# Kernel tuning notes

Hardware: AMD Instinct MI355X
Metric: run time of the kernel (lower is better)

## Reference

```python
import jax, jax.numpy as jnp
import numpy as np

B, S, H, E, F, TOP_K = 4, 2048, 512, 16, 1024, 2


def setup_inputs() -> dict:
    key = jax.random.key(0)
    k0, k1, k2, k3, k4 = jax.random.split(key, 5)
    scale = 0.02
    return {
        "inputs": jax.random.normal(k0, (B, S, H), dtype=jnp.float32),
        "router_w": jax.random.normal(k1, (E, H), dtype=jnp.float32) * scale,
        "gate_w": jax.random.normal(k2, (E, H, F), dtype=jnp.float32) * scale,
        "up_w": jax.random.normal(k3, (E, H, F), dtype=jnp.float32) * scale,
        "down_w": jax.random.normal(k4, (E, F, H), dtype=jnp.float32) * scale,
    }


def _moe_forward(inputs, router_w, gate_w, up_w, down_w):
    b, s, h = inputs.shape
    x = inputs.reshape(-1, h)                      # [T, H]
    T = x.shape[0]
    # --- routing: topk of logits then fp32 softmax over the k selected ---
    router_logits = x @ router_w.T                 # [T, E]
    top_vals, top_idx = jax.lax.top_k(router_logits, TOP_K)   # [T, K]
    weights = jax.nn.softmax(top_vals.astype(jnp.float32), axis=-1)  # [T, K]
    # dense combine weights: w[t, e] = routing weight if expert e selected else 0
    combine = jnp.zeros((T, router_w.shape[0]), jnp.float32)
    combine = combine.at[jnp.arange(T)[:, None], top_idx].set(weights)  # [T, E]

    # --- per-expert SwiGLU MLP, weighted combine (scan over experts) ---
    def step(acc, ew):
        wg, wu, wd, ce = ew                        # [H,F], [H,F], [F,H], [T]
        hid = jax.nn.silu(x @ wg) * (x @ wu)       # [T, F]
        y = hid @ wd                               # [T, H]
        return acc + ce[:, None] * y, None

    out0 = jnp.zeros_like(x)
    out, _ = jax.lax.scan(step, out0, (gate_w, up_w, down_w, combine.T))
    return out.reshape(b, s, h), router_logits, top_idx


def reference(inputs, router_w, gate_w, up_w, down_w):
    out, router_logits, selected_experts = _moe_forward(
        inputs, router_w, gate_w, up_w, down_w)
    return out
```

## Files before the change

### kernel.cpp

```cpp
#include <hip/hip_runtime.h>
#include <cstdint>
#include <cstddef>

#define T_TOK 8192
#define H_DIM 512
#define E_NUM 16
#define F_DIM 1024

typedef __bf16 bf16x8 __attribute__((ext_vector_type(8)));
typedef float f32x4 __attribute__((ext_vector_type(4)));

#define OFF_XBF  0UL
#define OFF_HID  8388608UL
#define OFF_GW   41943040UL
#define OFF_UW   58720256UL
#define OFF_DW   75497472UL
#define OFF_STOK 92274688UL
#define OFF_SW   92340224UL
#define OFF_TOPE 92405760UL
#define OFF_TOPW 92471296UL
#define OFF_CNT  92536832UL
#define OFF_CUR  92537856UL
#define OFF_OFFS 92538880UL

__device__ __forceinline__ unsigned short f2bf(float f) {
  union { float f; uint32_t u; } v; v.f = f;
  uint32_t r = v.u + 0x7fffu + ((v.u >> 16) & 1u);
  return (unsigned short)(r >> 16);
}

__device__ __forceinline__ void gld16(const void* g, void* l) {
  __builtin_amdgcn_global_load_lds(
      (const __attribute__((address_space(1))) unsigned int*)g,
      (__attribute__((address_space(3))) unsigned int*)l, 16, 0, 0);
}

__global__ __launch_bounds__(256) void k_router(
    const float* __restrict__ x, const float* __restrict__ rw,
    unsigned short* __restrict__ xbf, int* __restrict__ tope,
    float* __restrict__ topw) {
  const int wave = threadIdx.x >> 6, lane = threadIdx.x & 63;
  const int t = blockIdx.x * 4 + wave;
  const float4* xr = (const float4*)(x + (size_t)t * H_DIM + lane * 8);
  float4 a = xr[0], b = xr[1];
  float xi[8] = {a.x, a.y, a.z, a.w, b.x, b.y, b.z, b.w};
  uint4 o;
  o.x = (uint32_t)f2bf(xi[0]) | ((uint32_t)f2bf(xi[1]) << 16);
  o.y = (uint32_t)f2bf(xi[2]) | ((uint32_t)f2bf(xi[3]) << 16);
  o.z = (uint32_t)f2bf(xi[4]) | ((uint32_t)f2bf(xi[5]) << 16);
  o.w = (uint32_t)f2bf(xi[6]) | ((uint32_t)f2bf(xi[7]) << 16);
  *(uint4*)(xbf + (size_t)t * H_DIM + lane * 8) = o;
  float acc[E_NUM];
  #pragma unroll
  for (int e = 0; e < E_NUM; ++e) {
    const float4* wr = (const float4*)(rw + e * H_DIM + lane * 8);
    float4 wa = wr[0], wb = wr[1];
    acc[e] = xi[0]*wa.x + xi[1]*wa.y + xi[2]*wa.z + xi[3]*wa.w
           + xi[4]*wb.x + xi[5]*wb.y + xi[6]*wb.z + xi[7]*wb.w;
  }
  #pragma unroll
  for (int off = 1; off < 64; off <<= 1) {
    #pragma unroll
    for (int e = 0; e < E_NUM; ++e) acc[e] += __shfl_xor(acc[e], off);
  }
  if (lane == 0) {
    int e0 = 0; float v0 = acc[0];
    #pragma unroll
    for (int e = 1; e < E_NUM; ++e) if (acc[e] > v0) { v0 = acc[e]; e0 = e; }
    int e1 = -1; float v1 = -3.4e38f;
    #pragma unroll
    for (int e = 0; e < E_NUM; ++e) if (e != e0 && acc[e] > v1) { v1 = acc[e]; e1 = e; }
    float ee = __expf(v1 - v0);
    float inv = 1.0f / (1.0f + ee);
    tope[t*2]   = e0; tope[t*2+1] = e1;
    topw[t*2]   = inv; topw[t*2+1] = ee * inv;
  }
}

__global__ __launch_bounds__(256) void k_hist(
    const int* __restrict__ tope, int* __restrict__ counts) {
  __shared__ int lh[E_NUM];
  const int tid = threadIdx.x;
  if (tid < E_NUM) lh[tid] = 0;
  __syncthreads();
  atomicAdd(&lh[tope[blockIdx.x * 256 + tid]], 1);
  __syncthreads();
  if (tid < E_NUM) atomicAdd(&counts[tid * 16], lh[tid]);
}

__global__ void k_offsets(const int* __restrict__ counts, int* __restrict__ offs) {
  if (threadIdx.x == 0 && blockIdx.x == 0) {
    int s = 0;
    for (int e = 0; e < E_NUM; ++e) { offs[e] = s; s += counts[e * 16]; }
    offs[E_NUM] = s;
  }
}

__global__ __launch_bounds__(256) void k_scatter(
    const int* __restrict__ tope, const float* __restrict__ topw,
    const int* __restrict__ offs, int* __restrict__ cursors,
    int* __restrict__ stok, float* __restrict__ sw) {
  __shared__ int lh[E_NUM];
  __shared__ int lbase[E_NUM];
  const int tid = threadIdx.x;
  const int t = blockIdx.x * 256 + tid;
  if (tid < E_NUM) lh[tid] = 0;
  __syncthreads();
  int e0 = tope[t*2], e1 = tope[t*2+1];
  int r0 = atomicAdd(&lh[e0], 1);
  int r1 = atomicAdd(&lh[e1], 1);
  __syncthreads();
  if (tid < E_NUM) lbase[tid] = atomicAdd(&cursors[tid * 16], lh[tid]);
  __syncthreads();
  int s0 = offs[e0] + lbase[e0] + r0;
  int s1 = offs[e1] + lbase[e1] + r1;
  stok[s0] = t; sw[s0] = topw[t*2];
  stok[s1] = t; sw[s1] = topw[t*2+1];
}

__global__ __launch_bounds__(256) void k_prep_gu(
    const float* __restrict__ gw, const float* __restrict__ uw,
    unsigned short* __restrict__ gws, unsigned short* __restrict__ uws) {
  const int fx = blockIdx.x, kc = blockIdx.y, ez = blockIdx.z;
  const int e = ez >> 1;
  const float* src = ((ez & 1) ? uw : gw) + (size_t)e * H_DIM * F_DIM;
  unsigned short* dst = ((ez & 1) ? uws : gws);
  __shared__ float ls[32][132];
  const int tid = threadIdx.x;
  #pragma unroll
  for (int j = 0; j < 4; ++j) {
    int vi = tid + j * 256;
    int row = vi >> 5, c4 = (vi & 31) * 4;
    float4 v = *(const float4*)&src[(size_t)(kc*32 + row) * F_DIM + fx*128 + c4];
    ls[row][c4+0]=v.x; ls[row][c4+1]=v.y; ls[row][c4+2]=v.z; ls[row][c4+3]=v.w;
  }
  __syncthreads();
  size_t obase = (((size_t)e * 8 + fx) * 16 + kc) * 4096;
  #pragma unroll
  for (int j = 0; j < 2; ++j) {
    int oi = tid + j * 256;
    int f = oi >> 2, slot = oi & 3;
    int ks = ((slot ^ f) & 3) * 8;
    uint4 o;
    o.x = (uint32_t)f2bf(ls[ks+0][f]) | ((uint32_t)f2bf(ls[ks+1][f]) << 16);
    o.y = (uint32_t)f2bf(ls[ks+2][f]) | ((uint32_t)f2bf(ls[ks+3][f]) << 16);
    o.z = (uint32_t)f2bf(ls[ks+4][f]) | ((uint32_t)f2bf(ls[ks+5][f]) << 16);
    o.w = (uint32_t)f2bf(ls[ks+6][f]) | ((uint32_t)f2bf(ls[ks+7][f]) << 16);
    *(uint4*)&dst[obase + (size_t)oi * 8] = o;
  }
}

__global__ __launch_bounds__(256) void k_prep_dw(
    const float* __restrict__ dw, unsigned short* __restrict__ dws) {
  const int ht = blockIdx.x, kc = blockIdx.y, e = blockIdx.z;
  const float* src = dw + (size_t)e * F_DIM * H_DIM;
  __shared__ float ls[32][260];
  const int tid = threadIdx.x;
  #pragma unroll
  for (int j = 0; j < 8; ++j) {
    int vi = tid + j * 256;
    int row = vi >> 6, c4 = (vi & 63) * 4;
    float4 v = *(const float4*)&src[(size_t)(kc*32 + row) * H_DIM + ht*256 + c4];
    ls[row][c4+0]=v.x; ls[row][c4+1]=v.y; ls[row][c4+2]=v.z; ls[row][c4+3]=v.w;
  }
  __syncthreads();
  size_t obase = (((size_t)e * 2 + ht) * 32 + kc) * 8192;
  #pragma unroll
  for (int j = 0; j < 4; ++j) {
    int oi = tid + j * 256;
    int h = oi >> 2, slot = oi & 3;
    int ks = ((slot ^ h) & 3) * 8;
    uint4 o;
    o.x = (uint32_t)f2bf(ls[ks+0][h]) | ((uint32_t)f2bf(ls[ks+1][h]) << 16);
    o.y = (uint32_t)f2bf(ls[ks+2][h]) | ((uint32_t)f2bf(ls[ks+3][h]) << 16);
    o.z = (uint32_t)f2bf(ls[ks+4][h]) | ((uint32_t)f2bf(ls[ks+5][h]) << 16);
    o.w = (uint32_t)f2bf(ls[ks+6][h]) | ((uint32_t)f2bf(ls[ks+7][h]) << 16);
    *(uint4*)&dws[obase + (size_t)oi * 8] = o;
  }
}

__global__ __launch_bounds__(256, 2) void k_gateup(
    const unsigned short* __restrict__ xbf,
    const unsigned short* __restrict__ gws, const unsigned short* __restrict__ uws,
    const int* __restrict__ stok, const int* __restrict__ counts,
    const int* __restrict__ offs, unsigned short* __restrict__ hid) {
  const int e = blockIdx.z;
  const int cnt = counts[e * 16];
  const int t0 = blockIdx.y * 128;
  if (t0 >= cnt) return;
  const int base = offs[e];
  const int fx = blockIdx.x;

  __shared__ __align__(16) unsigned short sb[2][3][4096];

  const int tid = threadIdx.x;
  const int wave = tid >> 6, lane = tid & 63;
  const int l15 = lane & 15, hi = lane >> 4;
  const int wm = wave >> 1, wn = wave & 1;

  const int r0 = tid >> 2, slot = tid & 3;
  const int rr0 = min(t0 + r0, cnt - 1), rr1 = min(t0 + r0 + 64, cnt - 1);
  const char* sA0 = (const char*)xbf + (size_t)stok[base + rr0] * 1024 + ((slot ^ (r0 & 3)) * 16);
  const char* sA1 = (const char*)xbf + (size_t)stok[base + rr1] * 1024 + ((slot ^ (r0 & 3)) * 16);
  const char* sG = (const char*)gws + (((size_t)e * 8 + fx) * 16) * 8192 + tid * 16;
  const char* sU = (const char*)uws + (((size_t)e * 8 + fx) * 16) * 8192 + tid * 16;
  unsigned short* const dA = &sb[0][0][wave * 512];
  unsigned short* const dG = &sb[0][1][wave * 512];
  unsigned short* const dU = &sb[0][2][wave * 512];
  const int bufo = 3 * 4096;

  f32x4 accg[4][4] = {}; f32x4 accu[4][4] = {};

  #define STAGE_GU(b, kk) { \
    gld16(sA0 + (kk)*64, dA + (b)*bufo); \
    gld16(sA1 + (kk)*64, dA + (b)*bufo + 2048); \
    gld16(sG + (size_t)(kk)*8192, dG + (b)*bufo); \
    gld16(sG + (size_t)(kk)*8192 + 4096, dG + (b)*bufo + 2048); \
    gld16(sU + (size_t)(kk)*8192, dU + (b)*bufo); \
    gld16(sU + (size_t)(kk)*8192 + 4096, dU + (b)*bufo + 2048); }

  STAGE_GU(0, 0);
  __syncthreads();
  #pragma unroll 1
  for (int kk = 0; kk < 16; ++kk) {
    const int cur = kk & 1;
    if (kk < 15) STAGE_GU(cur ^ 1, kk + 1);
    const unsigned short* lA = &sb[cur][0][0];
    const unsigned short* lG = &sb[cur][1][0];
    const unsigned short* lU = &sb[cur][2][0];
    bf16x8 a[4], bg[4], bu[4];
    #pragma unroll
    for (int m = 0; m < 4; ++m) {
      int row = wm*64 + m*16 + l15;
      a[m] = *(const bf16x8*)((const char*)lA + row*64 + (((hi ^ row) & 3) << 4));
    }
    #pragma unroll
    for (int s = 0; s < 4; ++s) {
      int row = wn*64 + s*16 + l15;
      int o = row*64 + (((hi ^ row) & 3) << 4);
      bg[s] = *(const bf16x8*)((const char*)lG + o);
      bu[s] = *(const bf16x8*)((const char*)lU + o);
    }
    #pragma unroll
    for (int m = 0; m < 4; ++m)
      #pragma unroll
      for (int s = 0; s < 4; ++s) {
        accg[m][s] = __builtin_amdgcn_mfma_f32_16x16x32_bf16(a[m], bg[s], accg[m][s], 0, 0, 0);
        accu[m][s] = __builtin_amdgcn_mfma_f32_16x16x32_bf16(a[m], bu[s], accu[m][s], 0, 0, 0);
      }
    __syncthreads();
  }
  #undef STAGE_GU

  #pragma unroll
  for (int m = 0; m < 4; ++m)
    #pragma unroll
    for (int r = 0; r < 4; ++r) {
      int row = t0 + wm*64 + m*16 + hi*4 + r;
      if (row < cnt) {
        #pragma unroll
        for (int s = 0; s < 4; ++s) {
          float g = accg[m][s][r], u = accu[m][s][r];
          float h = g / (1.0f + __expf(-g)) * u;
          hid[(size_t)(base + row) * 1024 + fx*128 + wn*64 + s*16 + l15] = f2bf(h);
        }
      }
    }
}

__global__ __launch_bounds__(256, 2) void k_down(
    const unsigned short* __restrict__ hid, const unsigned short* __restrict__ dws,
    const int* __restrict__ stok, const float* __restrict__ sw,
    const int* __restrict__ counts, const int* __restrict__ offs,
    float* __restrict__ out) {
  const int e = blockIdx.z;
  const int cnt = counts[e * 16];
  const int t0 = blockIdx.y * 128;
  if (t0 >= cnt) return;
  const int base = offs[e];
  const int ht = blockIdx.x;

  __shared__ __align__(16) unsigned short sbA[2][4096];
  __shared__ __align__(16) unsigned short sbW[2][8192];

  const int tid = threadIdx.x;
  const int wave = tid >> 6, lane = tid & 63;
  const int l15 = lane & 15, hi = lane >> 4;
  const int wm = wave >> 1, wn = wave & 1;

  const int r0 = tid >> 2, slot = tid & 3;
  const int rr0 = min(t0 + r0, cnt - 1), rr1 = min(t0 + r0 + 64, cnt - 1);
  const char* sA0 = (const char*)hid + (size_t)(base + rr0) * 2048 + ((slot ^ (r0 & 3)) * 16);
  const char* sA1 = (const char*)hid + (size_t)(base + rr1) * 2048 + ((slot ^ (r0 & 3)) * 16);
  const char* sW = (const char*)dws + (((size_t)e * 2 + ht) * 32) * 16384 + tid * 16;
  unsigned short* const dA = &sbA[0][wave * 512];
  unsigned short* const dW = &sbW[0][wave * 512];

  f32x4 acc[4][8] = {};

  #define STAGE_DN(b, kk) { \
    gld16(sA0 + (kk)*64, dA + (b)*4096); \
    gld16(sA1 + (kk)*64, dA + (b)*4096 + 2048); \
    const char* w = sW + (size_t)(kk)*16384; \
    gld16(w,        dW + (b)*8192); \
    gld16(w + 4096, dW + (b)*8192 + 2048); \
    gld16(w + 8192, dW + (b)*8192 + 4096); \
    gld16(w + 12288, dW + (b)*8192 + 6144); }

  STAGE_DN(0, 0);
  __syncthreads();
  #pragma unroll 1
  for (int kk = 0; kk < 32; ++kk) {
    const int cur = kk & 1;
    if (kk < 31) STAGE_DN(cur ^ 1, kk + 1);
    const unsigned short* lA = &sbA[cur][0];
    const unsigned short* lW = &sbW[cur][0];
    bf16x8 a[4], b[8];
    #pragma unroll
    for (int m = 0; m < 4; ++m) {
      int row = wm*64 + m*16 + l15;
      a[m] = *(const bf16x8*)((const char*)lA + row*64 + (((hi ^ row) & 3) << 4));
    }
    #pragma unroll
    for (int s = 0; s < 8; ++s) {
      int row = wn*128 + s*16 + l15;
      b[s] = *(const bf16x8*)((const char*)lW + row*64 + (((hi ^ row) & 3) << 4));
    }
    #pragma unroll
    for (int m = 0; m < 4; ++m)
      #pragma unroll
      for (int s = 0; s < 8; ++s)
        acc[m][s] = __builtin_amdgcn_mfma_f32_16x16x32_bf16(a[m], b[s], acc[m][s], 0, 0, 0);
    __syncthreads();
  }
  #undef STAGE_DN

  #pragma unroll
  for (int m = 0; m < 4; ++m)
    #pragma unroll
    for (int r = 0; r < 4; ++r) {
      int row = t0 + wm*64 + m*16 + hi*4 + r;
      if (row < cnt) {
        int sl = base + row;
        int t = stok[sl];
        float w = sw[sl];
        float* orow = out + (size_t)t * H_DIM + ht*256 + wn*128;
        #pragma unroll
        for (int s = 0; s < 8; ++s)
          atomicAdd(&orow[s*16 + l15], w * acc[m][s][r]);
      }
    }
}

extern "C" void kernel_launch(void* const* d_in, const int* in_sizes, int n_in,
                              void* d_out, int out_size, void* d_ws, size_t ws_size,
                              hipStream_t stream) {
  const float* x  = (const float*)d_in[0];
  const float* rw = (const float*)d_in[1];
  const float* gw = (const float*)d_in[2];
  const float* uw = (const float*)d_in[3];
  const float* dw = (const float*)d_in[4];
  float* out = (float*)d_out;
  char* ws = (char*)d_ws;

  unsigned short* xbf = (unsigned short*)(ws + OFF_XBF);
  unsigned short* hid = (unsigned short*)(ws + OFF_HID);
  unsigned short* gws = (unsigned short*)(ws + OFF_GW);
  unsigned short* uws = (unsigned short*)(ws + OFF_UW);
  unsigned short* dws = (unsigned short*)(ws + OFF_DW);
  int*   stok    = (int*)(ws + OFF_STOK);
  float* swt     = (float*)(ws + OFF_SW);
  int*   tope    = (int*)(ws + OFF_TOPE);
  float* topw    = (float*)(ws + OFF_TOPW);
  int*   counts  = (int*)(ws + OFF_CNT);
  int*   cursors = (int*)(ws + OFF_CUR);
  int*   offs    = (int*)(ws + OFF_OFFS);

  hipMemsetAsync(ws + OFF_CNT, 0, 2048 + 128, stream);
  hipMemsetAsync(d_out, 0, (size_t)T_TOK * H_DIM * sizeof(float), stream);

  k_prep_gu<<<dim3(8, 16, 32), 256, 0, stream>>>(gw, uw, gws, uws);
  k_prep_dw<<<dim3(2, 32, 16), 256, 0, stream>>>(dw, dws);
  k_router<<<T_TOK / 4, 256, 0, stream>>>(x, rw, xbf, tope, topw);
  k_hist<<<T_TOK * 2 / 256, 256, 0, stream>>>(tope, counts);
  k_offsets<<<1, 64, 0, stream>>>(counts, offs);
  k_scatter<<<T_TOK / 256, 256, 0, stream>>>(tope, topw, offs, cursors, stok, swt);
  k_gateup<<<dim3(8, T_TOK * 2 / 128, E_NUM), 256, 0, stream>>>(
      xbf, gws, uws, stok, counts, offs, hid);
  k_down<<<dim3(2, T_TOK * 2 / 128, E_NUM), 256, 0, stream>>>(
      hid, dws, stok, swt, counts, offs, out);
}
```

Baseline: 172.0 us.

## Merge weight prep and router into one kernel; shrink down-proj M tile to 64

Combines the three preprocessing kernels (gate/up weight convert, down weight convert, router) into one launch dispatched by block index. This removes two launch gaps and lets the phases overlap on the GPU. The down-projection kernel now uses 64-token tiles, with each wave covering a 64-column slice instead of a 2x2 wave grid, and its occupancy hint goes from 2 to 3 blocks. That gives more blocks and better occupancy for uneven expert counts, at the cost of reloading the down weights twice as often per token.

```diff
diff --git a/kernel.cpp b/kernel.cpp
--- a/kernel.cpp
+++ b/kernel.cpp
@@ -35,45 +35,109 @@
       (__attribute__((address_space(3))) unsigned int*)l, 16, 0, 0);
 }
 
-__global__ __launch_bounds__(256) void k_router(
+__global__ __launch_bounds__(256) void k_pre(
     const float* __restrict__ x, const float* __restrict__ rw,
+    const float* __restrict__ gw, const float* __restrict__ uw,
+    const float* __restrict__ dw,
     unsigned short* __restrict__ xbf, int* __restrict__ tope,
-    float* __restrict__ topw) {
-  const int wave = threadIdx.x >> 6, lane = threadIdx.x & 63;
-  const int t = blockIdx.x * 4 + wave;
-  const float4* xr = (const float4*)(x + (size_t)t * H_DIM + lane * 8);
-  float4 a = xr[0], b = xr[1];
-  float xi[8] = {a.x, a.y, a.z, a.w, b.x, b.y, b.z, b.w};
-  uint4 o;
-  o.x = (uint32_t)f2bf(xi[0]) | ((uint32_t)f2bf(xi[1]) << 16);
-  o.y = (uint32_t)f2bf(xi[2]) | ((uint32_t)f2bf(xi[3]) << 16);
-  o.z = (uint32_t)f2bf(xi[4]) | ((uint32_t)f2bf(xi[5]) << 16);
-  o.w = (uint32_t)f2bf(xi[6]) | ((uint32_t)f2bf(xi[7]) << 16);
-  *(uint4*)(xbf + (size_t)t * H_DIM + lane * 8) = o;
-  float acc[E_NUM];
-  #pragma unroll
-  for (int e = 0; e < E_NUM; ++e) {
-    const float4* wr = (const float4*)(rw + e * H_DIM + lane * 8);
-    float4 wa = wr[0], wb = wr[1];
-    acc[e] = xi[0]*wa.x + xi[1]*wa.y + xi[2]*wa.z + xi[3]*wa.w
-           + xi[4]*wb.x + xi[5]*wb.y + xi[6]*wb.z + xi[7]*wb.w;
-  }
-  #pragma unroll
-  for (int off = 1; off < 64; off <<= 1) {
-    #pragma unroll
-    for (int e = 0; e < E_NUM; ++e) acc[e] += __shfl_xor(acc[e], off);
-  }
-  if (lane == 0) {
-    int e0 = 0; float v0 = acc[0];
-    #pragma unroll
-    for (int e = 1; e < E_NUM; ++e) if (acc[e] > v0) { v0 = acc[e]; e0 = e; }
-    int e1 = -1; float v1 = -3.4e38f;
-    #pragma unroll
-    for (int e = 0; e < E_NUM; ++e) if (e != e0 && acc[e] > v1) { v1 = acc[e]; e1 = e; }
-    float ee = __expf(v1 - v0);
-    float inv = 1.0f / (1.0f + ee);
-    tope[t*2]   = e0; tope[t*2+1] = e1;
-    topw[t*2]   = inv; topw[t*2+1] = ee * inv;
+    float* __restrict__ topw,
+    unsigned short* __restrict__ gws, unsigned short* __restrict__ uws,
+    unsigned short* __restrict__ dws) {
+  const int bid = blockIdx.x;
+  const int tid = threadIdx.x;
+  __shared__ float ls[32 * 260];
+
+  if (bid < 4096) {
+    const int fx = bid & 7, kc = (bid >> 3) & 15, ez = bid >> 7;
+    const int e = ez >> 1;
+    const float* src = ((ez & 1) ? uw : gw) + (size_t)e * H_DIM * F_DIM;
+    unsigned short* dst = ((ez & 1) ? uws : gws);
+    #pragma unroll
+    for (int j = 0; j < 4; ++j) {
+      int vi = tid + j * 256;
+      int row = vi >> 5, c4 = (vi & 31) * 4;
+      float4 v = *(const float4*)&src[(size_t)(kc*32 + row) * F_DIM + fx*128 + c4];
+      ls[row*132 + c4+0]=v.x; ls[row*132 + c4+1]=v.y;
+      ls[row*132 + c4+2]=v.z; ls[row*132 + c4+3]=v.w;
+    }
+    __syncthreads();
+    size_t obase = (((size_t)e * 8 + fx) * 16 + kc) * 4096;
+    #pragma unroll
+    for (int j = 0; j < 2; ++j) {
+      int oi = tid + j * 256;
+      int f = oi >> 2, slot = oi & 3;
+      int ks = ((slot ^ f) & 3) * 8;
+      uint4 o;
+      o.x = (uint32_t)f2bf(ls[(ks+0)*132 + f]) | ((uint32_t)f2bf(ls[(ks+1)*132 + f]) << 16);
+      o.y = (uint32_t)f2bf(ls[(ks+2)*132 + f]) | ((uint32_t)f2bf(ls[(ks+3)*132 + f]) << 16);
+      o.z = (uint32_t)f2bf(ls[(ks+4)*132 + f]) | ((uint32_t)f2bf(ls[(ks+5)*132 + f]) << 16);
+      o.w = (uint32_t)f2bf(ls[(ks+6)*132 + f]) | ((uint32_t)f2bf(ls[(ks+7)*132 + f]) << 16);
+      *(uint4*)&dst[obase + (size_t)oi * 8] = o;
+    }
+  } else if (bid < 5120) {
+    const int i = bid - 4096;
+    const int ht = i & 1, kc = (i >> 1) & 31, e = i >> 6;
+    const float* src = dw + (size_t)e * F_DIM * H_DIM;
+    #pragma unroll
+    for (int j = 0; j < 8; ++j) {
+      int vi = tid + j * 256;
+      int row = vi >> 6, c4 = (vi & 63) * 4;
+      float4 v = *(const float4*)&src[(size_t)(kc*32 + row) * H_DIM + ht*256 + c4];
+      ls[row*260 + c4+0]=v.x; ls[row*260 + c4+1]=v.y;
+      ls[row*260 + c4+2]=v.z; ls[row*260 + c4+3]=v.w;
+    }
+    __syncthreads();
+    size_t obase = (((size_t)e * 2 + ht) * 32 + kc) * 8192;
+    #pragma unroll
+    for (int j = 0; j < 4; ++j) {
+      int oi = tid + j * 256;
+      int h = oi >> 2, slot = oi & 3;
+      int ks = ((slot ^ h) & 3) * 8;
+      uint4 o;
+      o.x = (uint32_t)f2bf(ls[(ks+0)*260 + h]) | ((uint32_t)f2bf(ls[(ks+1)*260 + h]) << 16);
+      o.y = (uint32_t)f2bf(ls[(ks+2)*260 + h]) | ((uint32_t)f2bf(ls[(ks+3)*260 + h]) << 16);
+      o.z = (uint32_t)f2bf(ls[(ks+4)*260 + h]) | ((uint32_t)f2bf(ls[(ks+5)*260 + h]) << 16);
+      o.w = (uint32_t)f2bf(ls[(ks+6)*260 + h]) | ((uint32_t)f2bf(ls[(ks+7)*260 + h]) << 16);
+      *(uint4*)&dws[obase + (size_t)oi * 8] = o;
+    }
+  } else {
+    const int rb = bid - 5120;
+    const int wave = tid >> 6, lane = tid & 63;
+    const int t = rb * 4 + wave;
+    const float4* xr = (const float4*)(x + (size_t)t * H_DIM + lane * 8);
+    float4 a = xr[0], b = xr[1];
+    float xi[8] = {a.x, a.y, a.z, a.w, b.x, b.y, b.z, b.w};
+    uint4 o;
+    o.x = (uint32_t)f2bf(xi[0]) | ((uint32_t)f2bf(xi[1]) << 16);
+    o.y = (uint32_t)f2bf(xi[2]) | ((uint32_t)f2bf(xi[3]) << 16);
+    o.z = (uint32_t)f2bf(xi[4]) | ((uint32_t)f2bf(xi[5]) << 16);
+    o.w = (uint32_t)f2bf(xi[6]) | ((uint32_t)f2bf(xi[7]) << 16);
+    *(uint4*)(xbf + (size_t)t * H_DIM + lane * 8) = o;
+    float acc[E_NUM];
+    #pragma unroll
+    for (int e = 0; e < E_NUM; ++e) {
+      const float4* wr = (const float4*)(rw + e * H_DIM + lane * 8);
+      float4 wa = wr[0], wb = wr[1];
+      acc[e] = xi[0]*wa.x + xi[1]*wa.y + xi[2]*wa.z + xi[3]*wa.w
+             + xi[4]*wb.x + xi[5]*wb.y + xi[6]*wb.z + xi[7]*wb.w;
+    }
+    #pragma unroll
+    for (int off = 1; off < 64; off <<= 1) {
+      #pragma unroll
+      for (int e = 0; e < E_NUM; ++e) acc[e] += __shfl_xor(acc[e], off);
+    }
+    if (lane == 0) {
+      int e0 = 0; float v0 = acc[0];
+      #pragma unroll
+      for (int e = 1; e < E_NUM; ++e) if (acc[e] > v0) { v0 = acc[e]; e0 = e; }
+      int e1 = -1; float v1 = -3.4e38f;
+      #pragma unroll
+      for (int e = 0; e < E_NUM; ++e) if (e != e0 && acc[e] > v1) { v1 = acc[e]; e1 = e; }
+      float ee = __expf(v1 - v0);
+      float inv = 1.0f / (1.0f + ee);
+      tope[t*2]   = e0; tope[t*2+1] = e1;
+      topw[t*2]   = inv; topw[t*2+1] = ee * inv;
+    }
   }
 }
 
@@ -116,67 +180,6 @@
   int s1 = offs[e1] + lbase[e1] + r1;
   stok[s0] = t; sw[s0] = topw[t*2];
   stok[s1] = t; sw[s1] = topw[t*2+1];
-}
-
-__global__ __launch_bounds__(256) void k_prep_gu(
-    const float* __restrict__ gw, const float* __restrict__ uw,
-    unsigned short* __restrict__ gws, unsigned short* __restrict__ uws) {
-  const int fx = blockIdx.x, kc = blockIdx.y, ez = blockIdx.z;
-  const int e = ez >> 1;
-  const float* src = ((ez & 1) ? uw : gw) + (size_t)e * H_DIM * F_DIM;
-  unsigned short* dst = ((ez & 1) ? uws : gws);
-  __shared__ float ls[32][132];
-  const int tid = threadIdx.x;
-  #pragma unroll
-  for (int j = 0; j < 4; ++j) {
-    int vi = tid + j * 256;
-    int row = vi >> 5, c4 = (vi & 31) * 4;
-    float4 v = *(const float4*)&src[(size_t)(kc*32 + row) * F_DIM + fx*128 + c4];
-    ls[row][c4+0]=v.x; ls[row][c4+1]=v.y; ls[row][c4+2]=v.z; ls[row][c4+3]=v.w;
-  }
-  __syncthreads();
-  size_t obase = (((size_t)e * 8 + fx) * 16 + kc) * 4096;
-  #pragma unroll
-  for (int j = 0; j < 2; ++j) {
-    int oi = tid + j * 256;
-    int f = oi >> 2, slot = oi & 3;
-    int ks = ((slot ^ f) & 3) * 8;
-    uint4 o;
-    o.x = (uint32_t)f2bf(ls[ks+0][f]) | ((uint32_t)f2bf(ls[ks+1][f]) << 16);
-    o.y = (uint32_t)f2bf(ls[ks+2][f]) | ((uint32_t)f2bf(ls[ks+3][f]) << 16);
-    o.z = (uint32_t)f2bf(ls[ks+4][f]) | ((uint32_t)f2bf(ls[ks+5][f]) << 16);
-    o.w = (uint32_t)f2bf(ls[ks+6][f]) | ((uint32_t)f2bf(ls[ks+7][f]) << 16);
-    *(uint4*)&dst[obase + (size_t)oi * 8] = o;
-  }
-}
-
-__global__ __launch_bounds__(256) void k_prep_dw(
-    const float* __restrict__ dw, unsigned short* __restrict__ dws) {
-  const int ht = blockIdx.x, kc = blockIdx.y, e = blockIdx.z;
-  const float* src = dw + (size_t)e * F_DIM * H_DIM;
-  __shared__ float ls[32][260];
-  const int tid = threadIdx.x;
-  #pragma unroll
-  for (int j = 0; j < 8; ++j) {
-    int vi = tid + j * 256;
-    int row = vi >> 6, c4 = (vi & 63) * 4;
-    float4 v = *(const float4*)&src[(size_t)(kc*32 + row) * H_DIM + ht*256 + c4];
-    ls[row][c4+0]=v.x; ls[row][c4+1]=v.y; ls[row][c4+2]=v.z; ls[row][c4+3]=v.w;
-  }
-  __syncthreads();
-  size_t obase = (((size_t)e * 2 + ht) * 32 + kc) * 8192;
-  #pragma unroll
-  for (int j = 0; j < 4; ++j) {
-    int oi = tid + j * 256;
-    int h = oi >> 2, slot = oi & 3;
-    int ks = ((slot ^ h) & 3) * 8;
-    uint4 o;
-    o.x = (uint32_t)f2bf(ls[ks+0][h]) | ((uint32_t)f2bf(ls[ks+1][h]) << 16);
-    o.y = (uint32_t)f2bf(ls[ks+2][h]) | ((uint32_t)f2bf(ls[ks+3][h]) << 16);
-    o.z = (uint32_t)f2bf(ls[ks+4][h]) | ((uint32_t)f2bf(ls[ks+5][h]) << 16);
-    o.w = (uint32_t)f2bf(ls[ks+6][h]) | ((uint32_t)f2bf(ls[ks+7][h]) << 16);
-    *(uint4*)&dws[obase + (size_t)oi * 8] = o;
-  }
 }
 
 __global__ __launch_bounds__(256, 2) void k_gateup(
@@ -268,43 +271,40 @@
     }
 }
 
-__global__ __launch_bounds__(256, 2) void k_down(
+__global__ __launch_bounds__(256, 3) void k_down(
     const unsigned short* __restrict__ hid, const unsigned short* __restrict__ dws,
     const int* __restrict__ stok, const float* __restrict__ sw,
     const int* __restrict__ counts, const int* __restrict__ offs,
     float* __restrict__ out) {
   const int e = blockIdx.z;
   const int cnt = counts[e * 16];
-  const int t0 = blockIdx.y * 128;
+  const int t0 = blockIdx.y * 64;
   if (t0 >= cnt) return;
   const int base = offs[e];
   const int ht = blockIdx.x;
 
-  __shared__ __align__(16) unsigned short sbA[2][4096];
+  __shared__ __align__(16) unsigned short sbA[2][2048];
   __shared__ __align__(16) unsigned short sbW[2][8192];
 
   const int tid = threadIdx.x;
   const int wave = tid >> 6, lane = tid & 63;
   const int l15 = lane & 15, hi = lane >> 4;
-  const int wm = wave >> 1, wn = wave & 1;
 
   const int r0 = tid >> 2, slot = tid & 3;
-  const int rr0 = min(t0 + r0, cnt - 1), rr1 = min(t0 + r0 + 64, cnt - 1);
-  const char* sA0 = (const char*)hid + (size_t)(base + rr0) * 2048 + ((slot ^ (r0 & 3)) * 16);
-  const char* sA1 = (const char*)hid + (size_t)(base + rr1) * 2048 + ((slot ^ (r0 & 3)) * 16);
+  const int rr = min(t0 + r0, cnt - 1);
+  const char* sA = (const char*)hid + (size_t)(base + rr) * 2048 + ((slot ^ (r0 & 3)) * 16);
   const char* sW = (const char*)dws + (((size_t)e * 2 + ht) * 32) * 16384 + tid * 16;
   unsigned short* const dA = &sbA[0][wave * 512];
   unsigned short* const dW = &sbW[0][wave * 512];
 
-  f32x4 acc[4][8] = {};
+  f32x4 acc[4][4] = {};
 
   #define STAGE_DN(b, kk) { \
-    gld16(sA0 + (kk)*64, dA + (b)*4096); \
-    gld16(sA1 + (kk)*64, dA + (b)*4096 + 2048); \
+    gld16(sA + (kk)*64, dA + (b)*2048); \
     const char* w = sW + (size_t)(kk)*16384; \
-    gld16(w,        dW + (b)*8192); \
-    gld16(w + 4096, dW + (b)*8192 + 2048); \
-    gld16(w + 8192, dW + (b)*8192 + 4096); \
+    gld16(w,         dW + (b)*8192); \
+    gld16(w + 4096,  dW + (b)*8192 + 2048); \
+    gld16(w + 8192,  dW + (b)*8192 + 4096); \
     gld16(w + 12288, dW + (b)*8192 + 6144); }
 
   STAGE_DN(0, 0);
@@ -315,21 +315,21 @@
     if (kk < 31) STAGE_DN(cur ^ 1, kk + 1);
     const unsigned short* lA = &sbA[cur][0];
     const unsigned short* lW = &sbW[cur][0];
-    bf16x8 a[4], b[8];
+    bf16x8 a[4], b[4];
     #pragma unroll
     for (int m = 0; m < 4; ++m) {
-      int row = wm*64 + m*16 + l15;
+      int row = m*16 + l15;
       a[m] = *(const bf16x8*)((const char*)lA + row*64 + (((hi ^ row) & 3) << 4));
     }
     #pragma unroll
-    for (int s = 0; s < 8; ++s) {
-      int row = wn*128 + s*16 + l15;
+    for (int s = 0; s < 4; ++s) {
+      int row = wave*64 + s*16 + l15;
       b[s] = *(const bf16x8*)((const char*)lW + row*64 + (((hi ^ row) & 3) << 4));
     }
     #pragma unroll
     for (int m = 0; m < 4; ++m)
       #pragma unroll
-      for (int s = 0; s < 8; ++s)
+      for (int s = 0; s < 4; ++s)
         acc[m][s] = __builtin_amdgcn_mfma_f32_16x16x32_bf16(a[m], b[s], acc[m][s], 0, 0, 0);
     __syncthreads();
   }
@@ -339,14 +339,14 @@
   for (int m = 0; m < 4; ++m)
     #pragma unroll
     for (int r = 0; r < 4; ++r) {
-      int row = t0 + wm*64 + m*16 + hi*4 + r;
+      int row = t0 + m*16 + hi*4 + r;
       if (row < cnt) {
         int sl = base + row;
         int t = stok[sl];
         float w = sw[sl];
-        float* orow = out + (size_t)t * H_DIM + ht*256 + wn*128;
+        float* orow = out + (size_t)t * H_DIM + ht*256 + wave*64;
         #pragma unroll
-        for (int s = 0; s < 8; ++s)
+        for (int s = 0; s < 4; ++s)
           atomicAdd(&orow[s*16 + l15], w * acc[m][s][r]);
       }
     }
@@ -379,14 +379,12 @@
   hipMemsetAsync(ws + OFF_CNT, 0, 2048 + 128, stream);
   hipMemsetAsync(d_out, 0, (size_t)T_TOK * H_DIM * sizeof(float), stream);
 
-  k_prep_gu<<<dim3(8, 16, 32), 256, 0, stream>>>(gw, uw, gws, uws);
-  k_prep_dw<<<dim3(2, 32, 16), 256, 0, stream>>>(dw, dws);
-  k_router<<<T_TOK / 4, 256, 0, stream>>>(x, rw, xbf, tope, topw);
+  k_pre<<<7168, 256, 0, stream>>>(x, rw, gw, uw, dw, xbf, tope, topw, gws, uws, dws);
   k_hist<<<T_TOK * 2 / 256, 256, 0, stream>>>(tope, counts);
   k_offsets<<<1, 64, 0, stream>>>(counts, offs);
   k_scatter<<<T_TOK / 256, 256, 0, stream>>>(tope, topw, offs, cursors, stok, swt);
   k_gateup<<<dim3(8, T_TOK * 2 / 128, E_NUM), 256, 0, stream>>>(
       xbf, gws, uws, stok, counts, offs, hid);
-  k_down<<<dim3(2, T_TOK * 2 / 128, E_NUM), 256, 0, stream>>>(
+  k_down<<<dim3(2, T_TOK * 2 / 64, E_NUM), 256, 0, stream>>>(
       hid, dws, stok, swt, counts, offs, out);
 }
```

Result: no change. 172.9 us (+0.5%).
